# Kernel optimization log

Measured on AMD Instinct MI355X. Metric: run time of the kernel, lower is better.

Reference implementation:

```python
import jax, jax.numpy as jnp
import numpy as np

HEADS = 16


def setup_inputs() -> dict:
    key = jax.random.key(0)
    ks = jax.random.split(key, 5)
    n, s, d = 2, 2048, 1024
    return {
        "x": jax.random.normal(ks[0], (n, s, d), dtype=jnp.float32),
        "Wqkv": jax.random.normal(ks[1], (3 * d, d), dtype=jnp.float32) * (d ** -0.5),
        "bqkv": jax.random.normal(ks[2], (3 * d,), dtype=jnp.float32) * 0.02,
        "Wd": jax.random.normal(ks[3], (d, d), dtype=jnp.float32) * (d ** -0.5),
        "bd": jax.random.normal(ks[4], (d,), dtype=jnp.float32) * 0.02,
        "mask": 1,
    }


def reference(x, Wqkv, bqkv, Wd, bd, mask):
    n, s, d = x.shape
    h = HEADS
    hd = d // h
    qkv = x @ Wqkv.T + bqkv  # [n, s, 3d]
    q, k, v = jnp.split(qkv, 3, axis=-1)
    # [n, h, s, hd]
    q = q.reshape(n, s, h, hd).transpose(0, 2, 1, 3)
    k = k.reshape(n, s, h, hd).transpose(0, 2, 1, 3)
    v = v.reshape(n, s, h, hd).transpose(0, 2, 1, 3)
    scores = jnp.einsum("bhqd,bhkd->bhqk", q, k)
    if mask:
        causal = jnp.triu(jnp.ones((s, s), dtype=bool), k=1)
        scores = jnp.where(causal, -jnp.inf, scores)
    attn = jax.nn.softmax(scores / jnp.sqrt(jnp.float32(hd)), axis=-1)
    out = jnp.einsum("bhqk,bhkd->bhqd", attn, v)
    out = out.transpose(0, 2, 1, 3).reshape(n, s, d)
    return out @ Wd.T + bd
```

## Files before the change

kernel.cpp:

```cpp
#include <hip/hip_runtime.h>
#include <hip/hip_bf16.h>
#include <cstdint>
#include <cstddef>

typedef __attribute__((ext_vector_type(8))) short bf8_t;
typedef __attribute__((ext_vector_type(4))) float f4_t;

__device__ __forceinline__ unsigned short f2bf(float f) {
    union { float f; unsigned int u; } v; v.f = f;
    unsigned int u = v.u + 0x7FFFu + ((v.u >> 16) & 1u);
    return (unsigned short)(u >> 16);
}
__device__ __forceinline__ float bf2f(unsigned short s) {
    union { unsigned int u; float f; } v; v.u = ((unsigned int)s) << 16;
    return v.f;
}

__device__ __forceinline__ void gl_lds16(const void* g, void* l) {
    __builtin_amdgcn_global_load_lds(
        (const __attribute__((address_space(1))) unsigned int*)g,
        (__attribute__((address_space(3))) unsigned int*)l,
        16, 0, 0);
}

__global__ void cvt_kernel(const float* __restrict__ x,    unsigned short* __restrict__ xb,
                           const float* __restrict__ wq,   unsigned short* __restrict__ wqb,
                           const float* __restrict__ wd,   unsigned short* __restrict__ wdb) {
    int i = blockIdx.x * blockDim.x + threadIdx.x;
    const float* src; unsigned short* dst; int off;
    if (i < 1048576)       { src = x;  dst = xb;  off = i; }
    else if (i < 1835008)  { src = wq; dst = wqb; off = i - 1048576; }
    else                   { src = wd; dst = wdb; off = i - 1835008; }
    float4 f = ((const float4*)src)[off];
    ushort4 o;
    o.x = f2bf(f.x); o.y = f2bf(f.y); o.z = f2bf(f.z); o.w = f2bf(f.w);
    ((ushort4*)dst)[off] = o;
}

template<int MODE, int TM>
__device__ __forceinline__ void gemm_body(
    const unsigned short* __restrict__ A,
    const unsigned short* __restrict__ W,
    const float* __restrict__ bias,
    float* __restrict__ outf,
    unsigned short* __restrict__ qb,
    unsigned short* __restrict__ kb,
    unsigned short* __restrict__ vtb,
    int K, int Nn)
{
    constexpr int HM = TM / 2;
    constexpr int MB = HM / 16;
    constexpr int AI = TM / 32;
    constexpr int SSTG = (TM + 128) * 64;
    constexpr int SMEM = (MODE == 0 && SSTG < 128 * 136) ? 128 * 136 : SSTG;

    __shared__ unsigned short smem[SMEM];
    unsigned short* As = smem;
    unsigned short* Bs = smem + TM * 64;

    const int tid  = threadIdx.x;
    const int lane = tid & 63;
    const int w    = tid >> 6;
    const int wm   = w & 1;
    const int wn   = w >> 1;
    const int quad = lane >> 4;
    const int l16  = lane & 15;
    const int m0   = blockIdx.y * TM;
    const int n0   = blockIdx.x * 128;

    const int lrow = lane >> 3;
    const int lcol = ((lane & 7) ^ lrow) << 3;

    f4_t acc[MB][4];
    {
        f4_t z = {0.f, 0.f, 0.f, 0.f};
        #pragma unroll
        for (int i = 0; i < MB; ++i)
            #pragma unroll
            for (int j = 0; j < 4; ++j) acc[i][j] = z;
    }

    const unsigned short* Agp = A + (size_t)(m0 + w * (TM / 4) + lrow) * K + lcol;
    const unsigned short* Bgp = W + (size_t)(n0 + w * 32 + lrow) * K + lcol;
    unsigned short* lAp = &As[(w * (TM / 4)) * 64];
    unsigned short* lBp = &Bs[(w * 32) * 64];

    for (int kk = 0; kk < K; kk += 64) {
        __syncthreads();
        #pragma unroll
        for (int i = 0; i < AI; ++i)
            gl_lds16(Agp + (size_t)(i * 8) * K + kk, lAp + i * 8 * 64);
        #pragma unroll
        for (int i = 0; i < 4; ++i)
            gl_lds16(Bgp + (size_t)(i * 8) * K + kk, lBp + i * 8 * 64);
        __syncthreads();

        const int sw = l16 & 7;
        #pragma unroll
        for (int ks = 0; ks < 2; ++ks) {
            bf8_t af[MB], bfr[4];
            #pragma unroll
            for (int mb = 0; mb < MB; ++mb)
                af[mb] = *(const bf8_t*)&As[(wm * HM + mb * 16 + l16) * 64 + ((((ks << 2) | quad) ^ sw) << 3)];
            #pragma unroll
            for (int nb = 0; nb < 4; ++nb)
                bfr[nb] = *(const bf8_t*)&Bs[(wn * 64 + nb * 16 + l16) * 64 + ((((ks << 2) | quad) ^ sw) << 3)];
            #pragma unroll
            for (int mb = 0; mb < MB; ++mb)
                #pragma unroll
                for (int nb = 0; nb < 4; ++nb)
                    acc[mb][nb] = __builtin_amdgcn_mfma_f32_16x16x32_bf16(af[mb], bfr[nb], acc[mb][nb], 0, 0, 0);
        }
    }

    if (MODE == 0 && n0 >= 2048) {
        unsigned short* T = smem;
        __syncthreads();
        #pragma unroll
        for (int nb = 0; nb < 4; ++nb) {
            const int colL = wn * 64 + nb * 16 + l16;
            const float bc = bias[n0 + colL];
            #pragma unroll
            for (int mb = 0; mb < MB; ++mb) {
                const int rowL = wm * HM + mb * 16 + quad * 4;
                uint2 p;
                p.x = (unsigned int)f2bf(acc[mb][nb][0] + bc) |
                      ((unsigned int)f2bf(acc[mb][nb][1] + bc) << 16);
                p.y = (unsigned int)f2bf(acc[mb][nb][2] + bc) |
                      ((unsigned int)f2bf(acc[mb][nb][3] + bc) << 16);
                *(uint2*)&T[colL * 136 + rowL] = p;
            }
        }
        __syncthreads();
        const int trow  = tid >> 1;
        const int thalf = (tid & 1) << 6;
        const int head  = ((n0 - 2048) >> 6) + (trow >> 6);
        const int hdi   = trow & 63;
        const int bh    = ((m0 >> 11) << 4) + head;
        const int sq0   = (m0 & 2047) + thalf;
        unsigned short* dst = vtb + ((size_t)bh * 64 + hdi) * 2048 + sq0;
        const unsigned short* srcT = &T[trow * 136 + thalf];
        #pragma unroll
        for (int j = 0; j < 8; ++j)
            *(float4*)(dst + j * 8) = *(const float4*)(srcT + j * 8);
        return;
    }

    #pragma unroll
    for (int nb = 0; nb < 4; ++nb) {
        const int col = n0 + wn * 64 + nb * 16 + l16;
        const float bc = bias[col];
        const int within = col & 1023;
        const int head   = within >> 6;
        const int hdi    = within & 63;
        const bool isQ   = (col < 1024);
        #pragma unroll
        for (int mb = 0; mb < MB; ++mb) {
            #pragma unroll
            for (int r = 0; r < 4; ++r) {
                const int row = m0 + wm * HM + mb * 16 + quad * 4 + r;
                const float v = acc[mb][nb][r] + bc;
                if (MODE == 0) {
                    const int b  = row >> 11;
                    const int sq = row & 2047;
                    const int bh = b * 16 + head;
                    const unsigned short bv = f2bf(v);
                    if (isQ) qb[((size_t)bh * 2048 + sq) * 64 + hdi] = bv;
                    else     kb[((size_t)bh * 2048 + sq) * 64 + hdi] = bv;
                } else {
                    outf[(size_t)row * Nn + col] = v;
                }
            }
        }
    }
}

__global__ __launch_bounds__(256, 2) void qkv_gemm(
    const unsigned short* __restrict__ A, const unsigned short* __restrict__ W,
    const float* __restrict__ bias, unsigned short* __restrict__ qb,
    unsigned short* __restrict__ kb, unsigned short* __restrict__ vtb, int K, int Nn)
{
    gemm_body<0, 128>(A, W, bias, nullptr, qb, kb, vtb, K, Nn);
}

__global__ __launch_bounds__(256, 2) void proj_gemm(
    const unsigned short* __restrict__ A, const unsigned short* __restrict__ W,
    const float* __restrict__ bias, float* __restrict__ outf, int K, int Nn)
{
    gemm_body<1, 64>(A, W, bias, outf, nullptr, nullptr, nullptr, K, Nn);
}

__global__ __launch_bounds__(256, 4) void attn_kernel(
    const unsigned short* __restrict__ qg,
    const unsigned short* __restrict__ kg,
    const unsigned short* __restrict__ vg,
    unsigned short* __restrict__ ao,
    unsigned short* __restrict__ pO,
    float* __restrict__ pL)
{
    __shared__ unsigned short Ks[2][4096];
    __shared__ unsigned short Vs[2][4096];
    __shared__ unsigned short Ps[4096];

    const int tid  = threadIdx.x;
    const int lane = tid & 63;
    const int w    = tid >> 6;
    const int quad = lane >> 4;
    const int l16  = lane & 15;
    const int bx   = blockIdx.x;
    const int bh   = ((bx & 7) << 2) | ((bx >> 3) & 3);
    const int h    = (bx >> 5) & 1;
    const int jj   = bx >> 6;
    const int qtBig   = 31 - jj;
    const int qtSmall = jj;
    const int b    = bh >> 4;
    const int head = bh & 15;
    const int p0len = 32 - jj;
    const int t0 = h ? 17 : 0;
    const int t1 = h ? 33 : 17;

    const unsigned short* Qp = qg + (size_t)bh * 2048 * 64;
    const unsigned short* Kp = kg + (size_t)bh * 2048 * 64;
    const unsigned short* Vp = vg + (size_t)bh * 64 * 2048;

    const int srow = lane >> 3;
    const int scol = ((lane & 7) ^ srow) << 3;
    const unsigned short* kga = Kp + (size_t)(w * 16 + srow) * 64 + scol;
    const unsigned short* vga = Vp + (size_t)(w * 16 + srow) * 2048 + scol;
    const int sw = l16 & 7;

    auto stageKV = [&](int kt, int buf) {
        const int sk0 = kt << 6;
        gl_lds16(kga + (size_t)sk0 * 64,       &Ks[buf][w * 16 * 64]);
        gl_lds16(kga + (size_t)sk0 * 64 + 512, &Ks[buf][(w * 16 + 8) * 64]);
        gl_lds16(vga + sk0,                    &Vs[buf][w * 16 * 64]);
        gl_lds16(vga + sk0 + 8 * 2048,         &Vs[buf][(w * 16 + 8) * 64]);
    };

    bf8_t bones;
    {
        const short one = (l16 == 0) ? (short)0x3F80 : (short)0;
        #pragma unroll
        for (int j = 0; j < 8; ++j) bones[j] = one;
    }

    f4_t oacc[4];
    f4_t lacc;
    {
        f4_t z = {0.f, 0.f, 0.f, 0.f};
        #pragma unroll
        for (int j = 0; j < 4; ++j) oacc[j] = z;
        lacc = z;
    }

    bf8_t aq[2];
    {
        const int qt_init = (t0 >= p0len) ? qtSmall : qtBig;
        const size_t qrow = (size_t)(qt_init * 64 + w * 16 + l16) * 64;
        aq[0] = *(const bf8_t*)(Qp + qrow + quad * 8);
        aq[1] = *(const bf8_t*)(Qp + qrow + 32 + quad * 8);
    }

    auto flushPartial = [&]() {
        const int tb = (h << 9) + (bh << 4) + jj;
        unsigned short* po = pO + (size_t)tb * 4096;
        #pragma unroll
        for (int r = 0; r < 4; ++r) {
            const int row = w * 16 + quad * 4 + r;
            #pragma unroll
            for (int nb = 0; nb < 4; ++nb)
                po[row * 64 + nb * 16 + l16] = f2bf(oacc[nb][r]);
            if (l16 == 0) pL[tb * 64 + row] = lacc[r];
        }
    };

    {
        const int kt0 = (t0 >= p0len) ? (t0 - p0len) : t0;
        stageKV(kt0, t0 & 1);
    }

    for (int t = t0; t < t1; ++t) {
        const int buf = t & 1;
        __syncthreads();

        if (t + 1 < t1) {
            const int t2 = t + 1;
            stageKV((t2 >= p0len) ? (t2 - p0len) : t2, t2 & 1);
        }

        if (t == p0len) {
            flushPartial();
            f4_t z = {0.f, 0.f, 0.f, 0.f};
            #pragma unroll
            for (int j = 0; j < 4; ++j) oacc[j] = z;
            lacc = z;
            const size_t qrow = (size_t)(qtSmall * 64 + w * 16 + l16) * 64;
            aq[0] = *(const bf8_t*)(Qp + qrow + quad * 8);
            aq[1] = *(const bf8_t*)(Qp + qrow + 32 + quad * 8);
        }

        const bool ph1 = (t >= p0len);
        const int  kt  = ph1 ? (t - p0len) : t;
        const int  qtc = ph1 ? qtSmall : qtBig;
        const bool diag = (kt == qtc);

        f4_t sacc[4];
        {
            f4_t z = {0.f, 0.f, 0.f, 0.f};
            #pragma unroll
            for (int j = 0; j < 4; ++j) sacc[j] = z;
        }
        #pragma unroll
        for (int ks = 0; ks < 2; ++ks) {
            #pragma unroll
            for (int nb = 0; nb < 4; ++nb) {
                bf8_t bk = *(const bf8_t*)&Ks[buf][(nb * 16 + l16) * 64 + ((((ks << 2) | quad) ^ sw) << 3)];
                sacc[nb] = __builtin_amdgcn_mfma_f32_16x16x32_bf16(aq[ks], bk, sacc[nb], 0, 0, 0);
            }
        }

        if (!diag) {
            #pragma unroll
            for (int r = 0; r < 4; ++r) {
                const int rloc = (w << 4) + (quad << 2) + r;
                const int rk = rloc & 7;
                #pragma unroll
                for (int nb = 0; nb < 4; ++nb) {
                    union { float f; unsigned int u; } pv;
                    pv.f = exp2f(fmaf(sacc[nb][r], 0.18033688f, -20.197731f));
                    Ps[rloc * 64 + ((((nb << 1) | (l16 >> 3)) ^ rk) << 3) + (l16 & 7)] =
                        (unsigned short)(pv.u >> 16);
                }
            }
        } else {
            #pragma unroll
            for (int r = 0; r < 4; ++r) {
                const int rloc = (w << 4) + (quad << 2) + r;
                const int rk = rloc & 7;
                #pragma unroll
                for (int nb = 0; nb < 4; ++nb) {
                    float e = fmaf(sacc[nb][r], 0.18033688f, -20.197731f);
                    if (nb * 16 + l16 > rloc) e = -1e30f;
                    union { float f; unsigned int u; } pv;
                    pv.f = exp2f(e);
                    Ps[rloc * 64 + ((((nb << 1) | (l16 >> 3)) ^ rk) << 3) + (l16 & 7)] =
                        (unsigned short)(pv.u >> 16);
                }
            }
        }

        #pragma unroll
        for (int ks = 0; ks < 2; ++ks) {
            bf8_t ap = *(const bf8_t*)&Ps[(w * 16 + l16) * 64 + ((((ks << 2) | quad) ^ sw) << 3)];
            #pragma unroll
            for (int nb = 0; nb < 4; ++nb) {
                bf8_t bv = *(const bf8_t*)&Vs[buf][(nb * 16 + l16) * 64 + ((((ks << 2) | quad) ^ sw) << 3)];
                oacc[nb] = __builtin_amdgcn_mfma_f32_16x16x32_bf16(ap, bv, oacc[nb], 0, 0, 0);
            }
            lacc = __builtin_amdgcn_mfma_f32_16x16x32_bf16(ap, bones, lacc, 0, 0, 0);
        }
    }

    if (!h) {
        flushPartial();
    } else {
        #pragma unroll
        for (int r = 0; r < 4; ++r) {
            const float lsum = __shfl(lacc[r], lane & 48);
            const float rl = 1.f / lsum;
            const int sq = qtSmall * 64 + (w << 4) + (quad << 2) + r;
            #pragma unroll
            for (int nb = 0; nb < 4; ++nb) {
                const int dcol = head * 64 + nb * 16 + l16;
                ao[((size_t)(b * 2048 + sq)) * 1024 + dcol] = f2bf(oacc[nb][r] * rl);
            }
        }
    }
}

__global__ void merge_kernel(const unsigned short* __restrict__ pO,
                             const float* __restrict__ pL,
                             unsigned short* __restrict__ ao) {
    const int blk  = blockIdx.x;
    const int bh   = blk >> 4;
    const int jj   = blk & 15;
    const int b    = bh >> 4;
    const int head = bh & 15;
    const int qt   = 31 - jj;
    const int row  = threadIdx.x >> 2;
    const int c0   = (threadIdx.x & 3) << 4;

    const float l = pL[blk * 64 + row] + pL[(512 + blk) * 64 + row];
    const float rl = 1.f / l;
    const unsigned short* p0 = pO + (size_t)blk * 4096 + row * 64 + c0;
    const unsigned short* p1 = pO + (size_t)(512 + blk) * 4096 + row * 64 + c0;
    unsigned short* dst = ao + ((size_t)(b * 2048 + qt * 64 + row)) * 1024 + head * 64 + c0;
    #pragma unroll
    for (int j = 0; j < 16; ++j)
        dst[j] = f2bf((bf2f(p0[j]) + bf2f(p1[j])) * rl);
}

extern "C" void kernel_launch(void* const* d_in, const int* in_sizes, int n_in,
                              void* d_out, int out_size, void* d_ws, size_t ws_size,
                              hipStream_t stream) {
    const float* x    = (const float*)d_in[0];
    const float* Wqkv = (const float*)d_in[1];
    const float* bqkv = (const float*)d_in[2];
    const float* Wd   = (const float*)d_in[3];
    const float* bd   = (const float*)d_in[4];
    float* out = (float*)d_out;

    char* ws = (char*)d_ws;
    unsigned short* xb    = (unsigned short*)(ws);
    unsigned short* wqkvb = (unsigned short*)(ws + 8388608);
    unsigned short* wdb   = (unsigned short*)(ws + 14680064);
    unsigned short* qb2   = (unsigned short*)(ws + 16777216);
    unsigned short* kb2   = (unsigned short*)(ws + 25165824);
    unsigned short* vtb   = (unsigned short*)(ws + 33554432);
    unsigned short* pO    = (unsigned short*)(ws + 41943040);
    float*          pL    = (float*)(ws + 50331648);
    unsigned short* ao    = xb;

    cvt_kernel<<<8192, 256, 0, stream>>>(x, xb, Wqkv, wqkvb, Wd, wdb);

    qkv_gemm<<<dim3(24, 32), 256, 0, stream>>>(
        xb, wqkvb, bqkv, qb2, kb2, vtb, 1024, 3072);

    attn_kernel<<<1024, 256, 0, stream>>>(qb2, kb2, vtb, ao, pO, pL);

    merge_kernel<<<512, 256, 0, stream>>>(pO, pL, ao);

    proj_gemm<<<dim3(8, 64), 256, 0, stream>>>(
        ao, wdb, bd, out, 1024, 1024);
}
```

Before: 177.7 us.

## Double attention query tile to 128 rows per block for K/V reuse

The attention kernel now handles 128 query rows per block, 32 per wave in two 16-row sub-tiles, so each staged K/V tile is reused across twice as many queries. K and V fragments are hoisted into registers once per step. The causal pairing, split schedule and merge kernel are adjusted to the new tile sizes, and the grid is halved. This cuts LDS and global K/V traffic per query. In exchange it uses more registers and LDS, lowers occupancy, and gives fewer blocks to balance across CUs.

Result: no change. 175.1 us (-1.5%).

```diff
diff --git a/kernel.cpp b/kernel.cpp
--- a/kernel.cpp
+++ b/kernel.cpp
@@ -190,7 +190,7 @@
     gemm_body<1, 64>(A, W, bias, outf, nullptr, nullptr, nullptr, K, Nn);
 }
 
-__global__ __launch_bounds__(256, 4) void attn_kernel(
+__global__ __launch_bounds__(256, 2) void attn_kernel(
     const unsigned short* __restrict__ qg,
     const unsigned short* __restrict__ kg,
     const unsigned short* __restrict__ vg,
@@ -200,7 +200,7 @@
 {
     __shared__ unsigned short Ks[2][4096];
     __shared__ unsigned short Vs[2][4096];
-    __shared__ unsigned short Ps[4096];
+    __shared__ unsigned short Ps[8192];
 
     const int tid  = threadIdx.x;
     const int lane = tid & 63;
@@ -209,15 +209,16 @@
     const int l16  = lane & 15;
     const int bx   = blockIdx.x;
     const int bh   = ((bx & 7) << 2) | ((bx >> 3) & 3);
-    const int h    = (bx >> 5) & 1;
-    const int jj   = bx >> 6;
-    const int qtBig   = 31 - jj;
+    const int rest = bx >> 5;
+    const int jj   = rest & 7;
+    const int h    = rest >> 3;
+    const int qtBig   = 15 - jj;
     const int qtSmall = jj;
     const int b    = bh >> 4;
     const int head = bh & 15;
-    const int p0len = 32 - jj;
+    const int p0len = 32 - 2 * jj;
     const int t0 = h ? 17 : 0;
-    const int t1 = h ? 33 : 17;
+    const int t1 = h ? 34 : 17;
 
     const unsigned short* Qp = qg + (size_t)bh * 2048 * 64;
     const unsigned short* Kp = kg + (size_t)bh * 2048 * 64;
@@ -244,40 +245,45 @@
         for (int j = 0; j < 8; ++j) bones[j] = one;
     }
 
-    f4_t oacc[4];
-    f4_t lacc;
+    f4_t oacc[2][4];
+    f4_t lacc[2];
     {
         f4_t z = {0.f, 0.f, 0.f, 0.f};
         #pragma unroll
-        for (int j = 0; j < 4; ++j) oacc[j] = z;
-        lacc = z;
-    }
-
-    bf8_t aq[2];
-    {
-        const int qt_init = (t0 >= p0len) ? qtSmall : qtBig;
-        const size_t qrow = (size_t)(qt_init * 64 + w * 16 + l16) * 64;
-        aq[0] = *(const bf8_t*)(Qp + qrow + quad * 8);
-        aq[1] = *(const bf8_t*)(Qp + qrow + 32 + quad * 8);
-    }
+        for (int mb = 0; mb < 2; ++mb) {
+            #pragma unroll
+            for (int j = 0; j < 4; ++j) oacc[mb][j] = z;
+            lacc[mb] = z;
+        }
+    }
+
+    bf8_t aq[2][2];
+    auto loadQ = [&](int qt) {
+        const unsigned short* q0 = Qp + (size_t)(qt * 128 + w * 32 + l16) * 64 + quad * 8;
+        aq[0][0] = *(const bf8_t*)(q0);
+        aq[0][1] = *(const bf8_t*)(q0 + 32);
+        aq[1][0] = *(const bf8_t*)(q0 + 16 * 64);
+        aq[1][1] = *(const bf8_t*)(q0 + 16 * 64 + 32);
+    };
 
     auto flushPartial = [&]() {
-        const int tb = (h << 9) + (bh << 4) + jj;
-        unsigned short* po = pO + (size_t)tb * 4096;
-        #pragma unroll
-        for (int r = 0; r < 4; ++r) {
-            const int row = w * 16 + quad * 4 + r;
-            #pragma unroll
-            for (int nb = 0; nb < 4; ++nb)
-                po[row * 64 + nb * 16 + l16] = f2bf(oacc[nb][r]);
-            if (l16 == 0) pL[tb * 64 + row] = lacc[r];
-        }
+        const int tb = (h << 8) + (bh << 3) + jj;
+        unsigned short* po = pO + (size_t)tb * 8192;
+        #pragma unroll
+        for (int mb = 0; mb < 2; ++mb)
+            #pragma unroll
+            for (int r = 0; r < 4; ++r) {
+                const int row = w * 32 + mb * 16 + quad * 4 + r;
+                #pragma unroll
+                for (int nb = 0; nb < 4; ++nb)
+                    po[row * 64 + nb * 16 + l16] = f2bf(oacc[mb][nb][r]);
+                if (l16 == 0) pL[tb * 128 + row] = lacc[mb][r];
+            }
     };
 
-    {
-        const int kt0 = (t0 >= p0len) ? (t0 - p0len) : t0;
-        stageKV(kt0, t0 & 1);
-    }
+    loadQ(qtBig);
+
+    stageKV((t0 >= p0len) ? (t0 - p0len) : t0, t0 & 1);
 
     for (int t = t0; t < t1; ++t) {
         const int buf = t & 1;
@@ -292,89 +298,109 @@
             flushPartial();
             f4_t z = {0.f, 0.f, 0.f, 0.f};
             #pragma unroll
-            for (int j = 0; j < 4; ++j) oacc[j] = z;
-            lacc = z;
-            const size_t qrow = (size_t)(qtSmall * 64 + w * 16 + l16) * 64;
-            aq[0] = *(const bf8_t*)(Qp + qrow + quad * 8);
-            aq[1] = *(const bf8_t*)(Qp + qrow + 32 + quad * 8);
+            for (int mb = 0; mb < 2; ++mb) {
+                #pragma unroll
+                for (int j = 0; j < 4; ++j) oacc[mb][j] = z;
+                lacc[mb] = z;
+            }
+            loadQ(qtSmall);
         }
 
         const bool ph1 = (t >= p0len);
         const int  kt  = ph1 ? (t - p0len) : t;
         const int  qtc = ph1 ? qtSmall : qtBig;
-        const bool diag = (kt == qtc);
-
-        f4_t sacc[4];
-        {
-            f4_t z = {0.f, 0.f, 0.f, 0.f};
-            #pragma unroll
-            for (int j = 0; j < 4; ++j) sacc[j] = z;
-        }
-        #pragma unroll
-        for (int ks = 0; ks < 2; ++ks) {
-            #pragma unroll
-            for (int nb = 0; nb < 4; ++nb) {
-                bf8_t bk = *(const bf8_t*)&Ks[buf][(nb * 16 + l16) * 64 + ((((ks << 2) | quad) ^ sw) << 3)];
-                sacc[nb] = __builtin_amdgcn_mfma_f32_16x16x32_bf16(aq[ks], bk, sacc[nb], 0, 0, 0);
-            }
-        }
-
-        if (!diag) {
-            #pragma unroll
-            for (int r = 0; r < 4; ++r) {
-                const int rloc = (w << 4) + (quad << 2) + r;
-                const int rk = rloc & 7;
-                #pragma unroll
-                for (int nb = 0; nb < 4; ++nb) {
-                    union { float f; unsigned int u; } pv;
-                    pv.f = exp2f(fmaf(sacc[nb][r], 0.18033688f, -20.197731f));
-                    Ps[rloc * 64 + ((((nb << 1) | (l16 >> 3)) ^ rk) << 3) + (l16 & 7)] =
-                        (unsigned short)(pv.u >> 16);
+        const bool isD0 = (kt == 2 * qtc);
+        const bool isD1 = (kt == 2 * qtc + 1);
+        const bool diag = isD0 || isD1;
+        const int  koff = isD1 ? 64 : 0;
+
+        bf8_t bk[2][4];
+        #pragma unroll
+        for (int ks = 0; ks < 2; ++ks)
+            #pragma unroll
+            for (int nb = 0; nb < 4; ++nb)
+                bk[ks][nb] = *(const bf8_t*)&Ks[buf][(nb * 16 + l16) * 64 + ((((ks << 2) | quad) ^ sw) << 3)];
+
+        #pragma unroll
+        for (int mb = 0; mb < 2; ++mb) {
+            f4_t sacc[4];
+            {
+                f4_t z = {0.f, 0.f, 0.f, 0.f};
+                #pragma unroll
+                for (int j = 0; j < 4; ++j) sacc[j] = z;
+            }
+            #pragma unroll
+            for (int ks = 0; ks < 2; ++ks)
+                #pragma unroll
+                for (int nb = 0; nb < 4; ++nb)
+                    sacc[nb] = __builtin_amdgcn_mfma_f32_16x16x32_bf16(aq[mb][ks], bk[ks][nb], sacc[nb], 0, 0, 0);
+
+            if (!diag) {
+                #pragma unroll
+                for (int r = 0; r < 4; ++r) {
+                    const int rloc = w * 32 + mb * 16 + (quad << 2) + r;
+                    const int rk = rloc & 7;
+                    #pragma unroll
+                    for (int nb = 0; nb < 4; ++nb) {
+                        union { float f; unsigned int u; } pv;
+                        pv.f = exp2f(fmaf(sacc[nb][r], 0.18033688f, -20.197731f));
+                        Ps[rloc * 64 + ((((nb << 1) | (l16 >> 3)) ^ rk) << 3) + (l16 & 7)] =
+                            (unsigned short)(pv.u >> 16);
+                    }
                 }
-            }
-        } else {
-            #pragma unroll
-            for (int r = 0; r < 4; ++r) {
-                const int rloc = (w << 4) + (quad << 2) + r;
-                const int rk = rloc & 7;
-                #pragma unroll
-                for (int nb = 0; nb < 4; ++nb) {
-                    float e = fmaf(sacc[nb][r], 0.18033688f, -20.197731f);
-                    if (nb * 16 + l16 > rloc) e = -1e30f;
-                    union { float f; unsigned int u; } pv;
-                    pv.f = exp2f(e);
-                    Ps[rloc * 64 + ((((nb << 1) | (l16 >> 3)) ^ rk) << 3) + (l16 & 7)] =
-                        (unsigned short)(pv.u >> 16);
+            } else {
+                #pragma unroll
+                for (int r = 0; r < 4; ++r) {
+                    const int rloc = w * 32 + mb * 16 + (quad << 2) + r;
+                    const int rk = rloc & 7;
+                    #pragma unroll
+                    for (int nb = 0; nb < 4; ++nb) {
+                        float e = fmaf(sacc[nb][r], 0.18033688f, -20.197731f);
+                        if (nb * 16 + l16 + koff > rloc) e = -1e30f;
+                        union { float f; unsigned int u; } pv;
+                        pv.f = exp2f(e);
+                        Ps[rloc * 64 + ((((nb << 1) | (l16 >> 3)) ^ rk) << 3) + (l16 & 7)] =
+                            (unsigned short)(pv.u >> 16);
+                    }
                 }
             }
         }
 
-        #pragma unroll
-        for (int ks = 0; ks < 2; ++ks) {
-            bf8_t ap = *(const bf8_t*)&Ps[(w * 16 + l16) * 64 + ((((ks << 2) | quad) ^ sw) << 3)];
-            #pragma unroll
-            for (int nb = 0; nb < 4; ++nb) {
-                bf8_t bv = *(const bf8_t*)&Vs[buf][(nb * 16 + l16) * 64 + ((((ks << 2) | quad) ^ sw) << 3)];
-                oacc[nb] = __builtin_amdgcn_mfma_f32_16x16x32_bf16(ap, bv, oacc[nb], 0, 0, 0);
-            }
-            lacc = __builtin_amdgcn_mfma_f32_16x16x32_bf16(ap, bones, lacc, 0, 0, 0);
-        }
+        bf8_t bv[2][4];
+        #pragma unroll
+        for (int ks = 0; ks < 2; ++ks)
+            #pragma unroll
+            for (int nb = 0; nb < 4; ++nb)
+                bv[ks][nb] = *(const bf8_t*)&Vs[buf][(nb * 16 + l16) * 64 + ((((ks << 2) | quad) ^ sw) << 3)];
+
+        #pragma unroll
+        for (int mb = 0; mb < 2; ++mb)
+            #pragma unroll
+            for (int ks = 0; ks < 2; ++ks) {
+                bf8_t ap = *(const bf8_t*)&Ps[(w * 32 + mb * 16 + l16) * 64 + ((((ks << 2) | quad) ^ sw) << 3)];
+                #pragma unroll
+                for (int nb = 0; nb < 4; ++nb)
+                    oacc[mb][nb] = __builtin_amdgcn_mfma_f32_16x16x32_bf16(ap, bv[ks][nb], oacc[mb][nb], 0, 0, 0);
+                lacc[mb] = __builtin_amdgcn_mfma_f32_16x16x32_bf16(ap, bones, lacc[mb], 0, 0, 0);
+            }
     }
 
     if (!h) {
         flushPartial();
     } else {
         #pragma unroll
-        for (int r = 0; r < 4; ++r) {
-            const float lsum = __shfl(lacc[r], lane & 48);
-            const float rl = 1.f / lsum;
-            const int sq = qtSmall * 64 + (w << 4) + (quad << 2) + r;
-            #pragma unroll
-            for (int nb = 0; nb < 4; ++nb) {
-                const int dcol = head * 64 + nb * 16 + l16;
-                ao[((size_t)(b * 2048 + sq)) * 1024 + dcol] = f2bf(oacc[nb][r] * rl);
-            }
-        }
+        for (int mb = 0; mb < 2; ++mb)
+            #pragma unroll
+            for (int r = 0; r < 4; ++r) {
+                const float lsum = __shfl(lacc[mb][r], lane & 48);
+                const float rl = 1.f / lsum;
+                const int sq = qtSmall * 128 + w * 32 + mb * 16 + (quad << 2) + r;
+                #pragma unroll
+                for (int nb = 0; nb < 4; ++nb) {
+                    const int dcol = head * 64 + nb * 16 + l16;
+                    ao[((size_t)(b * 2048 + sq)) * 1024 + dcol] = f2bf(oacc[mb][nb][r] * rl);
+                }
+            }
     }
 }
 
@@ -382,21 +408,21 @@
                              const float* __restrict__ pL,
                              unsigned short* __restrict__ ao) {
     const int blk  = blockIdx.x;
-    const int bh   = blk >> 4;
-    const int jj   = blk & 15;
+    const int bh   = blk >> 3;
+    const int jj   = blk & 7;
     const int b    = bh >> 4;
     const int head = bh & 15;
-    const int qt   = 31 - jj;
-    const int row  = threadIdx.x >> 2;
-    const int c0   = (threadIdx.x & 3) << 4;
-
-    const float l = pL[blk * 64 + row] + pL[(512 + blk) * 64 + row];
+    const int qt   = 15 - jj;
+    const int row  = threadIdx.x >> 1;
+    const int c0   = (threadIdx.x & 1) << 5;
+
+    const float l = pL[blk * 128 + row] + pL[(256 + blk) * 128 + row];
     const float rl = 1.f / l;
-    const unsigned short* p0 = pO + (size_t)blk * 4096 + row * 64 + c0;
-    const unsigned short* p1 = pO + (size_t)(512 + blk) * 4096 + row * 64 + c0;
-    unsigned short* dst = ao + ((size_t)(b * 2048 + qt * 64 + row)) * 1024 + head * 64 + c0;
+    const unsigned short* p0 = pO + (size_t)blk * 8192 + row * 64 + c0;
+    const unsigned short* p1 = pO + (size_t)(256 + blk) * 8192 + row * 64 + c0;
+    unsigned short* dst = ao + ((size_t)(b * 2048 + qt * 128 + row)) * 1024 + head * 64 + c0;
     #pragma unroll
-    for (int j = 0; j < 16; ++j)
+    for (int j = 0; j < 32; ++j)
         dst[j] = f2bf((bf2f(p0[j]) + bf2f(p1[j])) * rl);
 }
 
@@ -426,9 +452,9 @@
     qkv_gemm<<<dim3(24, 32), 256, 0, stream>>>(
         xb, wqkvb, bqkv, qb2, kb2, vtb, 1024, 3072);
 
-    attn_kernel<<<1024, 256, 0, stream>>>(qb2, kb2, vtb, ao, pO, pL);
-
-    merge_kernel<<<512, 256, 0, stream>>>(pO, pL, ao);
+    attn_kernel<<<512, 256, 0, stream>>>(qb2, kb2, vtb, ao, pO, pL);
+
+    merge_kernel<<<256, 256, 0, stream>>>(pO, pL, ao);
 
     proj_gemm<<<dim3(8, 64), 256, 0, stream>>>(
         ao, wdb, bd, out, 1024, 1024);
```
